# Kernel optimization log

Hardware: AMD Instinct MI355X
Metric: run time of the kernel (lower is better)

## Reference

```python
import jax, jax.numpy as jnp
import numpy as np

N_VARS, N_CONS, N_EDGES = 200000, 100000, 1200000
VF, CF, H, R = 7, 5, 64, 2

def _glorot(k, shape):
    lim = 1.0 / np.sqrt(shape[-1])
    return jax.random.uniform(k, shape, jnp.float32, -lim, lim)

def setup_inputs() -> dict:
    key = jax.random.key(0)
    ks = jax.random.split(key, 20)
    return {
        "var_features": jax.random.normal(ks[0], (N_VARS, VF), jnp.float32),
        "con_features": jax.random.normal(ks[1], (N_CONS, CF), jnp.float32),
        "edge_var": jax.random.randint(ks[2], (N_EDGES,), 0, N_VARS, jnp.int32),
        "edge_con": jax.random.randint(ks[3], (N_EDGES,), 0, N_CONS, jnp.int32),
        # var encoder MLP (depth=1): in->hidden (tanh), hidden->out
        "W_ve1": _glorot(ks[4], (H, VF)), "b_ve1": jnp.zeros((H,), jnp.float32),
        "W_ve2": _glorot(ks[5], (H, H)),  "b_ve2": jnp.zeros((H,), jnp.float32),
        # con encoder MLP
        "W_ce1": _glorot(ks[6], (H, CF)), "b_ce1": jnp.zeros((H,), jnp.float32),
        "W_ce2": _glorot(ks[7], (H, H)),  "b_ce2": jnp.zeros((H,), jnp.float32),
        # per-round message linears, stacked over rounds
        "W_v2c": _glorot(ks[8], (R, H, H)), "b_v2c": jnp.zeros((R, H), jnp.float32),
        "W_c2v": _glorot(ks[9], (R, H, H)), "b_c2v": jnp.zeros((R, H), jnp.float32),
        # readout
        "W_ro": _glorot(ks[10], (1, H)), "b_ro": jnp.zeros((1,), jnp.float32),
    }

def reference(var_features, con_features, edge_var, edge_con,
              W_ve1, b_ve1, W_ve2, b_ve2,
              W_ce1, b_ce1, W_ce2, b_ce2,
              W_v2c, b_v2c, W_c2v, b_c2v,
              W_ro, b_ro):
    n_vars = var_features.shape[0]
    n_cons = con_features.shape[0]
    # encoders: eqx.nn.MLP(depth=1) = Linear -> tanh -> Linear
    h_var = jnp.tanh(var_features @ W_ve1.T + b_ve1) @ W_ve2.T + b_ve2  # (n_vars, H)
    h_con = jnp.tanh(con_features @ W_ce1.T + b_ce1) @ W_ce2.T + b_ce2  # (n_cons, H)
    n_rounds = W_v2c.shape[0]
    for r in range(n_rounds):
        # var -> con: gather, linear, scatter-add, tanh
        msg_v = h_var[edge_var] @ W_v2c[r].T + b_v2c[r]                 # (n_edges, H)
        agg_c = jax.ops.segment_sum(msg_v, edge_con, num_segments=n_cons)
        h_con = jnp.tanh(h_con + agg_c)
        # con -> var
        msg_c = h_con[edge_con] @ W_c2v[r].T + b_c2v[r]                 # (n_edges, H)
        agg_v = jax.ops.segment_sum(msg_c, edge_var, num_segments=n_vars)
        h_var = jnp.tanh(h_var + agg_v)
    scores = (h_var @ W_ro.T + b_ro).squeeze(-1)                        # (n_vars,)
    return scores
```

## Files before the change

### kernel.cpp

```cpp
#include <hip/hip_runtime.h>
#include <hip/hip_bf16.h>
#include <hip/hip_fp16.h>

#define WPB 4
#define SCAN_EPB 1024

#define CSB 384
#define BSH 7
#define BWID 128

typedef _Float16 h8 __attribute__((ext_vector_type(8)));
typedef float f32x4 __attribute__((ext_vector_type(4)));

__device__ __forceinline__ float bcast(float v, int i) {
  return __builtin_bit_cast(float, __builtin_amdgcn_readlane(__builtin_bit_cast(int, v), i));
}
__device__ __forceinline__ h8 h8zero() {
  h8 r;
#pragma unroll
  for (int j = 0; j < 8; ++j) r[j] = (_Float16)0;
  return r;
}
__device__ __forceinline__ h8 cvt8(float4 a, float4 b) {
  h8 r;
  r[0] = (_Float16)a.x; r[1] = (_Float16)a.y; r[2] = (_Float16)a.z; r[3] = (_Float16)a.w;
  r[4] = (_Float16)b.x; r[5] = (_Float16)b.y; r[6] = (_Float16)b.z; r[7] = (_Float16)b.w;
  return r;
}

template<int IN_F>
__global__ __launch_bounds__(256, 4) void encoder_mfma_kernel(
    const float* __restrict__ x,
    const float* __restrict__ W1, const float* __restrict__ b1,
    const h8* __restrict__ W2h, const float* __restrict__ b2,
    __half* __restrict__ out, int n_rows) {
  __shared__ _Float16 hlds[WPB][16][64];
  int t = threadIdx.x;
  int wave = t >> 6, lane = t & 63;
  int mm = lane & 15, fb = lane >> 4;

  float w1reg[IN_F];
#pragma unroll
  for (int j = 0; j < IN_F; ++j) w1reg[j] = W1[lane * IN_F + j];
  float b1v = b1[lane];

  h8 Bf[4][2];
  float bvt[4];
#pragma unroll
  for (int tt = 0; tt < 4; ++tt) {
#pragma unroll
    for (int s = 0; s < 2; ++s) Bf[tt][s] = W2h[(tt * 2 + s) * 64 + lane];
    bvt[tt] = b2[16 * tt + mm];
  }

  int c0 = ((fb ^ (mm & 7)) << 3);
  int c1 = (((4 + fb) ^ (mm & 7)) << 3);

  const int ntot = n_rows * IN_F;
  int stride16 = gridDim.x * WPB * 16;
  for (int rowb = (blockIdx.x * WPB + wave) * 16; rowb < n_rows; rowb += stride16) {
    int base = rowb * IN_F;
    float xa = 0.0f, xb = 0.0f;
    if (base + lane < ntot) xa = x[base + lane];
    if (base + 64 + lane < ntot) xb = x[base + 64 + lane];

#pragma unroll
    for (int r = 0; r < 16; ++r) {
      float h = b1v;
#pragma unroll
      for (int j = 0; j < IN_F; ++j) {
        int idx = r * IN_F + j;
        float xv;
        if (idx < 64) xv = bcast(xa, idx); else xv = bcast(xb, idx - 64);
        h += w1reg[j] * xv;
      }
      int sc = ((((lane >> 3) ^ (r & 7)) << 3) | (lane & 7));
      hlds[wave][r][sc] = (_Float16)tanhf(h);
    }

    h8 a0 = *(const h8*)&hlds[wave][mm][c0];
    h8 a1 = *(const h8*)&hlds[wave][mm][c1];

    f32x4 d[4];
#pragma unroll
    for (int tt = 0; tt < 4; ++tt) {
      f32x4 dz; dz[0] = bvt[tt]; dz[1] = bvt[tt]; dz[2] = bvt[tt]; dz[3] = bvt[tt];
      d[tt] = __builtin_amdgcn_mfma_f32_16x16x32_f16(a0, Bf[tt][0], dz, 0, 0, 0);
      d[tt] = __builtin_amdgcn_mfma_f32_16x16x32_f16(a1, Bf[tt][1], d[tt], 0, 0, 0);
    }

#pragma unroll
    for (int i = 0; i < 4; ++i) {
      int grow = rowb + fb * 4 + i;
      if (grow < n_rows) {
#pragma unroll
        for (int tt = 0; tt < 4; ++tt)
          out[(size_t)grow * 64 + 16 * tt + mm] = __float2half(d[tt][i]);
      }
    }
  }
}


__global__ __launch_bounds__(256) void bucket_hist_kernel(
    const int* __restrict__ ev, const int* __restrict__ ec,
    int* __restrict__ partial, int n_edges, int n_vars, int nbuckets) {
  extern __shared__ int cnt[];
  int t = threadIdx.x;
  for (int i = t; i < nbuckets; i += 256) cnt[i] = 0;
  __syncthreads();
  int chunk = (n_edges + CSB - 1) / CSB;
  int lo = blockIdx.x * chunk;
  int hi = lo + chunk; if (hi > n_edges) hi = n_edges;
  for (int e = lo + t; e < hi; e += 256) {
    int v = ev[e], c = ec[e];
    atomicAdd(&cnt[v >> BSH], 1);
    atomicAdd(&cnt[(n_vars + c) >> BSH], 1);
  }
  __syncthreads();
  for (int i = t; i < nbuckets; i += 256)
    partial[(size_t)i * CSB + blockIdx.x] = cnt[i];
}

__global__ __launch_bounds__(256) void bucket_place_kernel(
    const int* __restrict__ ev, const int* __restrict__ ec,
    const int* __restrict__ scanned, unsigned int* __restrict__ keypay,
    int n_edges, int n_vars, int nbuckets) {
  extern __shared__ int cur[];
  int t = threadIdx.x;
  for (int i = t; i < nbuckets; i += 256)
    cur[i] = scanned[(size_t)i * CSB + blockIdx.x];
  __syncthreads();
  int chunk = (n_edges + CSB - 1) / CSB;
  int lo = blockIdx.x * chunk;
  int hi = lo + chunk; if (hi > n_edges) hi = n_edges;
  for (int e = lo + t; e < hi; e += 256) {
    int v = ev[e], c = ec[e];
    int mc = n_vars + c;
    int s1 = atomicAdd(&cur[v >> BSH], 1);
    keypay[s1] = ((unsigned)(v & (BWID - 1)) << 25) | (unsigned)c;
    int s2 = atomicAdd(&cur[mc >> BSH], 1);
    keypay[s2] = ((unsigned)(mc & (BWID - 1)) << 25) | (unsigned)v;
  }
}

__global__ __launch_bounds__(256) void csr_fine_kernel(
    const unsigned int* __restrict__ keypay, const int* __restrict__ scanned,
    int* __restrict__ rp, int* __restrict__ esrc,
    __half* __restrict__ zvar, __half* __restrict__ zcon,
    int n_nodes, int nbuckets, int total) {
  __shared__ int cnt[BWID];
  __shared__ int pfx[BWID];
  __shared__ int cur[BWID];
  int j = blockIdx.x;
  int t = threadIdx.x;
  if (j == 0 && t < 64) {
    zvar[t] = __float2half(0.0f);
    zcon[t] = __float2half(0.0f);
  }
  int bstart = scanned[(size_t)j * CSB];
  int bend   = scanned[(size_t)(j + 1) * CSB];
  if (t < BWID) cnt[t] = 0;
  __syncthreads();
  for (int i = bstart + t; i < bend; i += 256)
    atomicAdd(&cnt[keypay[i] >> 25], 1);
  __syncthreads();
  if (t < BWID) pfx[t] = cnt[t];
  __syncthreads();
  for (int off = 1; off < BWID; off <<= 1) {
    int add = (t < BWID && t >= off) ? pfx[t - off] : 0;
    __syncthreads();
    if (t < BWID) pfx[t] += add;
    __syncthreads();
  }
  if (t < BWID) {
    int ex = pfx[t] - cnt[t];
    cur[t] = ex;
    int node = j * BWID + t;
    if (node < n_nodes) rp[node] = bstart + ex;
  }
  if (j == 0 && t == 0) rp[n_nodes] = total;
  __syncthreads();
  for (int i = bstart + t; i < bend; i += 256) {
    unsigned int kp = keypay[i];
    int off = atomicAdd(&cur[kp >> 25], 1);
    esrc[bstart + off] = (int)(kp & 0x1FFFFFFu);
  }
}

__global__ __launch_bounds__(256) void wcvt_all_kernel(
    const float* __restrict__ Wv2c, h8* __restrict__ Whv2c,
    const float* __restrict__ Wc2v, h8* __restrict__ Whc2v,
    const float* __restrict__ Wve2, h8* __restrict__ Whve2,
    const float* __restrict__ Wce2, h8* __restrict__ Whce2,
    int R512) {
  int tid = blockIdx.x * 256 + threadIdx.x;
  const float* W;
  h8* Wh;
  int local;
  if (tid < R512)                { W = Wv2c; Wh = Whv2c; local = tid; }
  else if (tid < 2 * R512)       { W = Wc2v; Wh = Whc2v; local = tid - R512; }
  else if (tid < 2 * R512 + 512) { W = Wve2; Wh = Whve2; local = tid - 2 * R512; }
  else if (tid < 2 * R512 + 1024){ W = Wce2; Wh = Whce2; local = tid - 2 * R512 - 512; }
  else return;
  int l = local & 63;
  int f = (local >> 6) & 7;
  int r = local >> 9;
  int tt = f >> 1, s = f & 1;
  const float* wp = W + (size_t)r * 4096 + (size_t)(16 * tt + (l & 15)) * 64
                    + 32 * s + 8 * (l >> 4);
  Wh[local] = cvt8(*(const float4*)wp, *(const float4*)(wp + 4));
}

__global__ __launch_bounds__(256) void scan_blocks_kernel(
    const int* __restrict__ in, int* __restrict__ out,
    int* __restrict__ bsums, int n) {
  __shared__ int s[256];
  int t = threadIdx.x;
  int base = blockIdx.x * SCAN_EPB + t * 4;
  int v[4]; int local = 0;
#pragma unroll
  for (int j = 0; j < 4; ++j) {
    int idx = base + j;
    v[j] = (idx < n) ? in[idx] : 0;
    local += v[j];
  }
  s[t] = local;
  __syncthreads();
  for (int off = 1; off < 256; off <<= 1) {
    int val = (t >= off) ? s[t - off] : 0;
    __syncthreads();
    s[t] += val;
    __syncthreads();
  }
  int run = s[t] - local;
#pragma unroll
  for (int j = 0; j < 4; ++j) {
    int idx = base + j;
    if (idx < n) out[idx] = run;
    run += v[j];
  }
  if (t == 255) bsums[blockIdx.x] = s[255];
}

__global__ __launch_bounds__(256) void scan_sums_kernel(int* __restrict__ bsums, int nb) {
  __shared__ int s[256];
  int t = threadIdx.x;
  int base = t * 4;
  int v[4]; int local = 0;
#pragma unroll
  for (int j = 0; j < 4; ++j) {
    int idx = base + j;
    v[j] = (idx < nb) ? bsums[idx] : 0;
    local += v[j];
  }
  s[t] = local;
  __syncthreads();
  for (int off = 1; off < 256; off <<= 1) {
    int val = (t >= off) ? s[t - off] : 0;
    __syncthreads();
    s[t] += val;
    __syncthreads();
  }
  int run = s[t] - local;
#pragma unroll
  for (int j = 0; j < 4; ++j) {
    int idx = base + j;
    if (idx < nb) bsums[idx] = run;
    run += v[j];
  }
}

__global__ __launch_bounds__(256) void scan_add_kernel(
    int* __restrict__ out, const int* __restrict__ bsums, int n, int total) {
  int t = threadIdx.x;
  int base = blockIdx.x * SCAN_EPB + t * 4;
  int add = bsums[blockIdx.x];
#pragma unroll
  for (int j = 0; j < 4; ++j) {
    int idx = base + j;
    if (idx < n) out[idx] += add;
  }
  if (blockIdx.x == 0 && t == 0) out[n] = total;
}

template<bool RO>
__global__ __launch_bounds__(256, 6) void fused_mfma_kernel(
    __half* __restrict__ hdst, const __half* __restrict__ hsrc,
    const int* __restrict__ rp, const int* __restrict__ esrc,
    const h8* __restrict__ Wh, const float* __restrict__ b,
    const float* __restrict__ Wro, const float* __restrict__ bro,
    float* __restrict__ scores, int n_rows, int zrow) {
  int t = threadIdx.x;
  int wave = t >> 6, lane = t & 63;
  int mm = lane & 15;
  int fb = lane >> 4;

  float brov = RO ? bro[0] : 0.0f;

  const float4* rows4 = (const float4*)hsrc;

  int stride16 = gridDim.x * WPB * 16;
  for (int rowb = (blockIdx.x * WPB + wave) * 16; rowb < n_rows; rowb += stride16) {
    int mrow = rowb + mm;
    int mc = (mrow < n_rows) ? mrow : n_rows - 1;
    int p = rp[mc], end = rp[mc + 1];
    float degf = (float)(end - p);

    h8 a0 = h8zero(), a1 = h8zero();

    int s0, s1, s2, s3;
    {
      bool v0 = p < end, v1 = p + 1 < end, v2 = p + 2 < end, v3 = p + 3 < end;
      s0 = esrc[v0 ? p : 0];     s0 = v0 ? s0 : zrow;
      s1 = esrc[v1 ? p + 1 : 0]; s1 = v1 ? s1 : zrow;
      s2 = esrc[v2 ? p + 2 : 0]; s2 = v2 ? s2 : zrow;
      s3 = esrc[v3 ? p + 3 : 0]; s3 = v3 ? s3 : zrow;
    }

    while (__any(p < end)) {
      float4 q0a = rows4[(size_t)s0 * 8 + fb];
      float4 q0b = rows4[(size_t)s0 * 8 + 4 + fb];
      float4 q1a = rows4[(size_t)s1 * 8 + fb];
      float4 q1b = rows4[(size_t)s1 * 8 + 4 + fb];
      float4 q2a = rows4[(size_t)s2 * 8 + fb];
      float4 q2b = rows4[(size_t)s2 * 8 + 4 + fb];
      float4 q3a = rows4[(size_t)s3 * 8 + fb];
      float4 q3b = rows4[(size_t)s3 * 8 + 4 + fb];

      int np = p + 4;
      {
        bool w0 = np < end, w1 = np + 1 < end, w2 = np + 2 < end, w3 = np + 3 < end;
        int u0 = esrc[w0 ? np : 0];     s0 = w0 ? u0 : zrow;
        int u1 = esrc[w1 ? np + 1 : 0]; s1 = w1 ? u1 : zrow;
        int u2 = esrc[w2 ? np + 2 : 0]; s2 = w2 ? u2 : zrow;
        int u3 = esrc[w3 ? np + 3 : 0]; s3 = w3 ? u3 : zrow;
      }

      a0 += __builtin_bit_cast(h8, q0a);
      a1 += __builtin_bit_cast(h8, q0b);
      a0 += __builtin_bit_cast(h8, q1a);
      a1 += __builtin_bit_cast(h8, q1b);
      a0 += __builtin_bit_cast(h8, q2a);
      a1 += __builtin_bit_cast(h8, q2b);
      a0 += __builtin_bit_cast(h8, q3a);
      a1 += __builtin_bit_cast(h8, q3b);
      p = np;
    }

    int zoff = 0;
    asm volatile("" : "+v"(zoff));
    const h8* Whb = Wh + zoff;
    const float* bb = b + zoff;
    const float* wrob = RO ? (Wro + zoff) : nullptr;

    float pr[4] = {0.f, 0.f, 0.f, 0.f};
#pragma unroll
    for (int h = 0; h < 2; ++h) {
      __builtin_amdgcn_sched_barrier(0);
      h8 Bf[2][2];
      float bvt[2], wrot[2];
#pragma unroll
      for (int s = 0; s < 2; ++s) {
        int tt = 2 * h + s;
#pragma unroll
        for (int ks = 0; ks < 2; ++ks)
          Bf[s][ks] = Whb[(tt * 2 + ks) * 64 + lane];
        bvt[s] = bb[16 * tt + mm];
        wrot[s] = RO ? wrob[16 * tt + mm] : 0.0f;
      }

      f32x4 d[2];
#pragma unroll
      for (int s = 0; s < 2; ++s) {
        f32x4 dz; dz[0] = 0.f; dz[1] = 0.f; dz[2] = 0.f; dz[3] = 0.f;
        d[s] = __builtin_amdgcn_mfma_f32_16x16x32_f16(a0, Bf[s][0], dz, 0, 0, 0);
        d[s] = __builtin_amdgcn_mfma_f32_16x16x32_f16(a1, Bf[s][1], d[s], 0, 0, 0);
      }

#pragma unroll
      for (int i = 0; i < 4; ++i) {
        float deg_i = __shfl(degf, fb * 4 + i, 64);
        int grow = rowb + fb * 4 + i;
        bool ok = grow < n_rows;
#pragma unroll
        for (int s = 0; s < 2; ++s) {
          int tt = 2 * h + s;
          size_t addr = (size_t)grow * 64 + 16 * tt + mm;
          float hold = ok ? __half2float(hdst[addr]) : 0.0f;
          float hv = tanhf(hold + bvt[s] * deg_i + d[s][i]);
          if (RO) {
            pr[i] += hv * wrot[s];
          } else {
            if (ok) hdst[addr] = __float2half(hv);
          }
        }
      }
    }

    if (RO) {
#pragma unroll
      for (int i = 0; i < 4; ++i) {
        float pv = pr[i];
        pv += __shfl_xor(pv, 1, 64);
        pv += __shfl_xor(pv, 2, 64);
        pv += __shfl_xor(pv, 4, 64);
        pv += __shfl_xor(pv, 8, 64);
        int grow = rowb + fb * 4 + i;
        if (mm == 0 && grow < n_rows) scores[grow] = pv + brov;
      }
    }
  }
}

static inline int rowgrid16(int n) {
  int want = (n + WPB * 16 - 1) / (WPB * 16);
  return want < 2048 ? want : 2048;
}

extern "C" void kernel_launch(void* const* d_in, const int* in_sizes, int n_in,
                              void* d_out, int out_size, void* d_ws, size_t ws_size,
                              hipStream_t stream) {
  const float* vf    = (const float*)d_in[0];
  const float* cf    = (const float*)d_in[1];
  const int*   ev    = (const int*)d_in[2];
  const int*   ec    = (const int*)d_in[3];
  const float* W_ve1 = (const float*)d_in[4];
  const float* b_ve1 = (const float*)d_in[5];
  const float* W_ve2 = (const float*)d_in[6];
  const float* b_ve2 = (const float*)d_in[7];
  const float* W_ce1 = (const float*)d_in[8];
  const float* b_ce1 = (const float*)d_in[9];
  const float* W_ce2 = (const float*)d_in[10];
  const float* b_ce2 = (const float*)d_in[11];
  const float* W_v2c = (const float*)d_in[12];
  const float* b_v2c = (const float*)d_in[13];
  const float* W_c2v = (const float*)d_in[14];
  const float* b_c2v = (const float*)d_in[15];
  const float* W_ro  = (const float*)d_in[16];
  const float* b_ro  = (const float*)d_in[17];

  const int n_vars  = in_sizes[0] / 7;
  const int n_cons  = in_sizes[1] / 5;
  const int n_edges = in_sizes[2];
  const int R       = in_sizes[12] / (64 * 64);
  const int n_nodes = n_vars + n_cons;

  char* p = (char*)d_ws;
  __half* h_var = (__half*)p; p += ((size_t)n_vars + 1) * 64 * 2;
  __half* h_con = (__half*)p; p += ((size_t)n_cons + 1) * 64 * 2;
  int*   rp     = (int*)p;   p += (size_t)(n_nodes + 1) * 4;
  int*   esrc   = (int*)p;   p += (size_t)2 * n_edges * 4;
  int*   bsums  = (int*)p;   p += 1024 * 4;
  h8*    wh_v2c = (h8*)p;    p += (size_t)R * 512 * 16;
  h8*    wh_c2v = (h8*)p;    p += (size_t)R * 512 * 16;
  h8*    wh_ve2 = (h8*)p;    p += (size_t)512 * 16;
  h8*    wh_ce2 = (h8*)p;    p += (size_t)512 * 16;

  const int nbuckets = (n_nodes + BWID - 1) >> BSH;
  const int nP = nbuckets * CSB;
  int* partial = (int*)h_var;
  int* scanned = partial + (size_t)(nP + 1);
  unsigned int* keypay = (unsigned int*)h_con;

  const int nb2 = (nP + SCAN_EPB - 1) / SCAN_EPB;

  bucket_hist_kernel<<<CSB, 256, nbuckets * 4, stream>>>(
      ev, ec, partial, n_edges, n_vars, nbuckets);

  {
    int total = 2 * R * 512 + 1024;
    wcvt_all_kernel<<<(total + 255) / 256, 256, 0, stream>>>(
        W_v2c, wh_v2c, W_c2v, wh_c2v, W_ve2, wh_ve2, W_ce2, wh_ce2, R * 512);
  }

  scan_blocks_kernel<<<nb2, 256, 0, stream>>>(partial, scanned, bsums, nP);
  scan_sums_kernel<<<1, 256, 0, stream>>>(bsums, nb2);
  scan_add_kernel<<<nb2, 256, 0, stream>>>(scanned, bsums, nP, 2 * n_edges);

  bucket_place_kernel<<<CSB, 256, nbuckets * 4, stream>>>(
      ev, ec, scanned, keypay, n_edges, n_vars, nbuckets);
  csr_fine_kernel<<<nbuckets, 256, 0, stream>>>(
      keypay, scanned, rp, esrc,
      h_var + (size_t)n_vars * 64, h_con + (size_t)n_cons * 64,
      n_nodes, nbuckets, 2 * n_edges);

  encoder_mfma_kernel<7><<<rowgrid16(n_vars), 256, 0, stream>>>(
      vf, W_ve1, b_ve1, wh_ve2, b_ve2, h_var, n_vars);
  encoder_mfma_kernel<5><<<rowgrid16(n_cons), 256, 0, stream>>>(
      cf, W_ce1, b_ce1, wh_ce2, b_ce2, h_con, n_cons);

  for (int r = 0; r < R; ++r) {
    fused_mfma_kernel<false><<<rowgrid16(n_cons), 256, 0, stream>>>(
        h_con, h_var, rp + n_vars, esrc,
        wh_v2c + (size_t)r * 512, b_v2c + (size_t)r * 64,
        nullptr, nullptr, nullptr, n_cons, n_vars);
    if (r == R - 1) {
      fused_mfma_kernel<true><<<rowgrid16(n_vars), 256, 0, stream>>>(
          h_var, h_con, rp, esrc,
          wh_c2v + (size_t)r * 512, b_c2v + (size_t)r * 64,
          W_ro, b_ro, (float*)d_out, n_vars, n_cons);
    } else {
      fused_mfma_kernel<false><<<rowgrid16(n_vars), 256, 0, stream>>>(
          h_var, h_con, rp, esrc,
          wh_c2v + (size_t)r * 512, b_c2v + (size_t)r * 64,
          nullptr, nullptr, nullptr, n_vars, n_cons);
    }
  }
}
```

Measured before the change: 369.1 us.

## Sort nodes by degree so each 16-row MFMA tile has uniform degree

Adds a counting sort of nodes by in-degree (a histogram kernel, a prefix scan and a placement kernel) that builds a permutation for variables and constraints separately. The fused message-passing kernel now handles rows in permuted order, so the 16 rows sharing a wave's gather loop have similar degree. This is meant to cut divergence, since the loop runs until the highest-degree row in the tile is done. In exchange it adds five extra launches, an indirect perm lookup per row, and scattered hdst and score writes that lose the locality of contiguous row order.

```diff
diff --git a/kernel.cpp b/kernel.cpp
--- a/kernel.cpp
+++ b/kernel.cpp
@@ -8,6 +8,9 @@
 #define CSB 384
 #define BSH 7
 #define BWID 128
+
+#define DNB 128
+#define DBINS 1024
 
 typedef _Float16 h8 __attribute__((ext_vector_type(8)));
 typedef float f32x4 __attribute__((ext_vector_type(4)));
@@ -185,6 +188,46 @@
     unsigned int kp = keypay[i];
     int off = atomicAdd(&cur[kp >> 25], 1);
     esrc[bstart + off] = (int)(kp & 0x1FFFFFFu);
+  }
+}
+
+__global__ __launch_bounds__(256) void deg_hist_kernel(
+    const int* __restrict__ rp, int* __restrict__ dpartial,
+    int n_nodes, int n_vars) {
+  __shared__ int cnt[DBINS];
+  int t = threadIdx.x;
+  for (int i = t; i < DBINS; i += 256) cnt[i] = 0;
+  __syncthreads();
+  int chunk = (n_nodes + DNB - 1) / DNB;
+  int lo = blockIdx.x * chunk;
+  int hi = lo + chunk; if (hi > n_nodes) hi = n_nodes;
+  for (int n = lo + t; n < hi; n += 256) {
+    int deg = rp[n + 1] - rp[n];
+    int bin = (n < n_vars ? 0 : 512) + (deg < 511 ? deg : 511);
+    atomicAdd(&cnt[bin], 1);
+  }
+  __syncthreads();
+  for (int i = t; i < DBINS; i += 256)
+    dpartial[(size_t)i * DNB + blockIdx.x] = cnt[i];
+}
+
+__global__ __launch_bounds__(256) void deg_place_kernel(
+    const int* __restrict__ rp, const int* __restrict__ dscanned,
+    int* __restrict__ perm, int n_nodes, int n_vars) {
+  __shared__ int cur[DBINS];
+  int t = threadIdx.x;
+  for (int i = t; i < DBINS; i += 256)
+    cur[i] = dscanned[(size_t)i * DNB + blockIdx.x];
+  __syncthreads();
+  int chunk = (n_nodes + DNB - 1) / DNB;
+  int lo = blockIdx.x * chunk;
+  int hi = lo + chunk; if (hi > n_nodes) hi = n_nodes;
+  for (int n = lo + t; n < hi; n += 256) {
+    int deg = rp[n + 1] - rp[n];
+    bool isv = n < n_vars;
+    int bin = (isv ? 0 : 512) + (deg < 511 ? deg : 511);
+    int slot = atomicAdd(&cur[bin], 1);
+    perm[slot] = isv ? n : (n - n_vars);
   }
 }
 
@@ -288,6 +331,7 @@
 __global__ __launch_bounds__(256, 6) void fused_mfma_kernel(
     __half* __restrict__ hdst, const __half* __restrict__ hsrc,
     const int* __restrict__ rp, const int* __restrict__ esrc,
+    const int* __restrict__ perm,
     const h8* __restrict__ Wh, const float* __restrict__ b,
     const float* __restrict__ Wro, const float* __restrict__ bro,
     float* __restrict__ scores, int n_rows, int zrow) {
@@ -302,8 +346,9 @@
 
   int stride16 = gridDim.x * WPB * 16;
   for (int rowb = (blockIdx.x * WPB + wave) * 16; rowb < n_rows; rowb += stride16) {
-    int mrow = rowb + mm;
-    int mc = (mrow < n_rows) ? mrow : n_rows - 1;
+    int lrow = rowb + mm;
+    int lc = (lrow < n_rows) ? lrow : n_rows - 1;
+    int mc = perm[lc];
     int p = rp[mc], end = rp[mc + 1];
     float degf = (float)(end - p);
 
@@ -381,12 +426,12 @@
 #pragma unroll
       for (int i = 0; i < 4; ++i) {
         float deg_i = __shfl(degf, fb * 4 + i, 64);
-        int grow = rowb + fb * 4 + i;
-        bool ok = grow < n_rows;
+        int arow = __shfl(mc, fb * 4 + i, 64);
+        bool ok = (rowb + fb * 4 + i) < n_rows;
 #pragma unroll
         for (int s = 0; s < 2; ++s) {
           int tt = 2 * h + s;
-          size_t addr = (size_t)grow * 64 + 16 * tt + mm;
+          size_t addr = (size_t)arow * 64 + 16 * tt + mm;
           float hold = ok ? __half2float(hdst[addr]) : 0.0f;
           float hv = tanhf(hold + bvt[s] * deg_i + d[s][i]);
           if (RO) {
@@ -406,8 +451,9 @@
         pv += __shfl_xor(pv, 2, 64);
         pv += __shfl_xor(pv, 4, 64);
         pv += __shfl_xor(pv, 8, 64);
-        int grow = rowb + fb * 4 + i;
-        if (mm == 0 && grow < n_rows) scores[grow] = pv + brov;
+        int arow = __shfl(mc, fb * 4 + i, 64);
+        bool ok = (rowb + fb * 4 + i) < n_rows;
+        if (mm == 0 && ok) scores[arow] = pv + brov;
       }
     }
   }
@@ -456,14 +502,19 @@
   h8*    wh_c2v = (h8*)p;    p += (size_t)R * 512 * 16;
   h8*    wh_ve2 = (h8*)p;    p += (size_t)512 * 16;
   h8*    wh_ce2 = (h8*)p;    p += (size_t)512 * 16;
+  int*   perm   = (int*)p;   p += (size_t)n_nodes * 4;
 
   const int nbuckets = (n_nodes + BWID - 1) >> BSH;
   const int nP = nbuckets * CSB;
   int* partial = (int*)h_var;
   int* scanned = partial + (size_t)(nP + 1);
   unsigned int* keypay = (unsigned int*)h_con;
+  const int nP2 = DBINS * DNB;
+  int* dpartial = (int*)h_var;
+  int* dscanned = dpartial + (size_t)(nP2 + 1);
 
   const int nb2 = (nP + SCAN_EPB - 1) / SCAN_EPB;
+  const int nb3 = (nP2 + SCAN_EPB - 1) / SCAN_EPB;
 
   bucket_hist_kernel<<<CSB, 256, nbuckets * 4, stream>>>(
       ev, ec, partial, n_edges, n_vars, nbuckets);
@@ -485,6 +536,12 @@
       h_var + (size_t)n_vars * 64, h_con + (size_t)n_cons * 64,
       n_nodes, nbuckets, 2 * n_edges);
 
+  deg_hist_kernel<<<DNB, 256, 0, stream>>>(rp, dpartial, n_nodes, n_vars);
+  scan_blocks_kernel<<<nb3, 256, 0, stream>>>(dpartial, dscanned, bsums, nP2);
+  scan_sums_kernel<<<1, 256, 0, stream>>>(bsums, nb3);
+  scan_add_kernel<<<nb3, 256, 0, stream>>>(dscanned, bsums, nP2, n_nodes);
+  deg_place_kernel<<<DNB, 256, 0, stream>>>(rp, dscanned, perm, n_nodes, n_vars);
+
   encoder_mfma_kernel<7><<<rowgrid16(n_vars), 256, 0, stream>>>(
       vf, W_ve1, b_ve1, wh_ve2, b_ve2, h_var, n_vars);
   encoder_mfma_kernel<5><<<rowgrid16(n_cons), 256, 0, stream>>>(
@@ -492,17 +549,17 @@
 
   for (int r = 0; r < R; ++r) {
     fused_mfma_kernel<false><<<rowgrid16(n_cons), 256, 0, stream>>>(
-        h_con, h_var, rp + n_vars, esrc,
+        h_con, h_var, rp + n_vars, esrc, perm + n_vars,
         wh_v2c + (size_t)r * 512, b_v2c + (size_t)r * 64,
         nullptr, nullptr, nullptr, n_cons, n_vars);
     if (r == R - 1) {
       fused_mfma_kernel<true><<<rowgrid16(n_vars), 256, 0, stream>>>(
-          h_var, h_con, rp, esrc,
+          h_var, h_con, rp, esrc, perm,
           wh_c2v + (size_t)r * 512, b_c2v + (size_t)r * 64,
           W_ro, b_ro, (float*)d_out, n_vars, n_cons);
     } else {
       fused_mfma_kernel<false><<<rowgrid16(n_vars), 256, 0, stream>>>(
-          h_var, h_con, rp, esrc,
+          h_var, h_con, rp, esrc, perm,
           wh_c2v + (size_t)r * 512, b_c2v + (size_t)r * 64,
           nullptr, nullptr, nullptr, n_vars, n_cons);
     }
```

After: 376.0 us. Within noise of the previous version (+1.8%).

## Sort rows by degree within buckets to balance per-wave gather loops

Applied to the files above, without the earlier changes.

In the CSR build kernel, each node gets a rank by degree inside its 128-node bucket, and a permutation is written separately for variables and constraints. The fused message kernels process rows in permuted order, so the 16 rows in each MFMA tile have similar degrees and the wave's __any loop wastes fewer iterations. Rows are now written back to scattered addresses taken from the permutation. The message kernels also launch an uncapped grid instead of capping it at 2048 blocks. The costs are an O(128) ranking loop per thread in csr_fine, one extra indirection per row, and less coalesced output writes.

```diff
diff --git a/kernel.cpp b/kernel.cpp
--- a/kernel.cpp
+++ b/kernel.cpp
@@ -146,9 +146,9 @@
 
 __global__ __launch_bounds__(256) void csr_fine_kernel(
     const unsigned int* __restrict__ keypay, const int* __restrict__ scanned,
-    int* __restrict__ rp, int* __restrict__ esrc,
+    int* __restrict__ rp, int* __restrict__ esrc, int* __restrict__ perm,
     __half* __restrict__ zvar, __half* __restrict__ zcon,
-    int n_nodes, int nbuckets, int total) {
+    int n_nodes, int n_vars, int nbuckets, int total) {
   __shared__ int cnt[BWID];
   __shared__ int pfx[BWID];
   __shared__ int cur[BWID];
@@ -177,7 +177,23 @@
     int ex = pfx[t] - cnt[t];
     cur[t] = ex;
     int node = j * BWID + t;
-    if (node < n_nodes) rp[node] = bstart + ex;
+    if (node < n_nodes) {
+      rp[node] = bstart + ex;
+      bool isv = node < n_vars;
+      int mydeg = cnt[t];
+      int rank = 0;
+      for (int u = 0; u < BWID; ++u) {
+        int un = j * BWID + u;
+        if (un >= n_nodes) break;
+        if ((un < n_vars) == isv) {
+          int ud = cnt[u];
+          if (ud > mydeg || (ud == mydeg && u < t)) ++rank;
+        }
+      }
+      int vbase = j * BWID;
+      int cbase = (j * BWID > n_vars) ? (j * BWID) : n_vars;
+      perm[(isv ? vbase : cbase) + rank] = isv ? node : (node - n_vars);
+    }
   }
   if (j == 0 && t == 0) rp[n_nodes] = total;
   __syncthreads();
@@ -288,6 +304,7 @@
 __global__ __launch_bounds__(256, 6) void fused_mfma_kernel(
     __half* __restrict__ hdst, const __half* __restrict__ hsrc,
     const int* __restrict__ rp, const int* __restrict__ esrc,
+    const int* __restrict__ perm,
     const h8* __restrict__ Wh, const float* __restrict__ b,
     const float* __restrict__ Wro, const float* __restrict__ bro,
     float* __restrict__ scores, int n_rows, int zrow) {
@@ -302,8 +319,9 @@
 
   int stride16 = gridDim.x * WPB * 16;
   for (int rowb = (blockIdx.x * WPB + wave) * 16; rowb < n_rows; rowb += stride16) {
-    int mrow = rowb + mm;
-    int mc = (mrow < n_rows) ? mrow : n_rows - 1;
+    int lrow = rowb + mm;
+    int lc = (lrow < n_rows) ? lrow : n_rows - 1;
+    int mc = perm[lc];
     int p = rp[mc], end = rp[mc + 1];
     float degf = (float)(end - p);
 
@@ -381,12 +399,12 @@
 #pragma unroll
       for (int i = 0; i < 4; ++i) {
         float deg_i = __shfl(degf, fb * 4 + i, 64);
-        int grow = rowb + fb * 4 + i;
-        bool ok = grow < n_rows;
+        int arow = __shfl(mc, fb * 4 + i, 64);
+        bool ok = (rowb + fb * 4 + i) < n_rows;
 #pragma unroll
         for (int s = 0; s < 2; ++s) {
           int tt = 2 * h + s;
-          size_t addr = (size_t)grow * 64 + 16 * tt + mm;
+          size_t addr = (size_t)arow * 64 + 16 * tt + mm;
           float hold = ok ? __half2float(hdst[addr]) : 0.0f;
           float hv = tanhf(hold + bvt[s] * deg_i + d[s][i]);
           if (RO) {
@@ -406,16 +424,20 @@
         pv += __shfl_xor(pv, 2, 64);
         pv += __shfl_xor(pv, 4, 64);
         pv += __shfl_xor(pv, 8, 64);
-        int grow = rowb + fb * 4 + i;
-        if (mm == 0 && grow < n_rows) scores[grow] = pv + brov;
-      }
-    }
-  }
-}
-
-static inline int rowgrid16(int n) {
+        int arow = __shfl(mc, fb * 4 + i, 64);
+        bool ok = (rowb + fb * 4 + i) < n_rows;
+        if (mm == 0 && ok) scores[arow] = pv + brov;
+      }
+    }
+  }
+}
+
+static inline int rowgrid16cap(int n) {
   int want = (n + WPB * 16 - 1) / (WPB * 16);
   return want < 2048 ? want : 2048;
+}
+static inline int rowgrid16full(int n) {
+  return (n + WPB * 16 - 1) / (WPB * 16);
 }
 
 extern "C" void kernel_launch(void* const* d_in, const int* in_sizes, int n_in,
@@ -456,6 +478,7 @@
   h8*    wh_c2v = (h8*)p;    p += (size_t)R * 512 * 16;
   h8*    wh_ve2 = (h8*)p;    p += (size_t)512 * 16;
   h8*    wh_ce2 = (h8*)p;    p += (size_t)512 * 16;
+  int*   perm   = (int*)p;   p += (size_t)n_nodes * 4;
 
   const int nbuckets = (n_nodes + BWID - 1) >> BSH;
   const int nP = nbuckets * CSB;
@@ -481,28 +504,28 @@
   bucket_place_kernel<<<CSB, 256, nbuckets * 4, stream>>>(
       ev, ec, scanned, keypay, n_edges, n_vars, nbuckets);
   csr_fine_kernel<<<nbuckets, 256, 0, stream>>>(
-      keypay, scanned, rp, esrc,
+      keypay, scanned, rp, esrc, perm,
       h_var + (size_t)n_vars * 64, h_con + (size_t)n_cons * 64,
-      n_nodes, nbuckets, 2 * n_edges);
-
-  encoder_mfma_kernel<7><<<rowgrid16(n_vars), 256, 0, stream>>>(
+      n_nodes, n_vars, nbuckets, 2 * n_edges);
+
+  encoder_mfma_kernel<7><<<rowgrid16cap(n_vars), 256, 0, stream>>>(
       vf, W_ve1, b_ve1, wh_ve2, b_ve2, h_var, n_vars);
-  encoder_mfma_kernel<5><<<rowgrid16(n_cons), 256, 0, stream>>>(
+  encoder_mfma_kernel<5><<<rowgrid16cap(n_cons), 256, 0, stream>>>(
       cf, W_ce1, b_ce1, wh_ce2, b_ce2, h_con, n_cons);
 
   for (int r = 0; r < R; ++r) {
-    fused_mfma_kernel<false><<<rowgrid16(n_cons), 256, 0, stream>>>(
-        h_con, h_var, rp + n_vars, esrc,
+    fused_mfma_kernel<false><<<rowgrid16full(n_cons), 256, 0, stream>>>(
+        h_con, h_var, rp + n_vars, esrc, perm + n_vars,
         wh_v2c + (size_t)r * 512, b_v2c + (size_t)r * 64,
         nullptr, nullptr, nullptr, n_cons, n_vars);
     if (r == R - 1) {
-      fused_mfma_kernel<true><<<rowgrid16(n_vars), 256, 0, stream>>>(
-          h_var, h_con, rp, esrc,
+      fused_mfma_kernel<true><<<rowgrid16full(n_vars), 256, 0, stream>>>(
+          h_var, h_con, rp, esrc, perm,
           wh_c2v + (size_t)r * 512, b_c2v + (size_t)r * 64,
           W_ro, b_ro, (float*)d_out, n_vars, n_cons);
     } else {
-      fused_mfma_kernel<false><<<rowgrid16(n_vars), 256, 0, stream>>>(
-          h_var, h_con, rp, esrc,
+      fused_mfma_kernel<false><<<rowgrid16full(n_vars), 256, 0, stream>>>(
+          h_var, h_con, rp, esrc, perm,
           wh_c2v + (size_t)r * 512, b_c2v + (size_t)r * 64,
           nullptr, nullptr, nullptr, n_vars, n_cons);
     }
```

Result: slower. 390.6 us (+5.8%).
